# Kernel optimization log

Hardware: AMD Instinct MI355X
Metric: run time of the kernel (lower is better)

Reference implementation:

```python
import jax, jax.numpy as jnp
import numpy as np

D_MODEL = 1024
STATE_DIM = 128


def setup_inputs() -> dict:
    key = jax.random.key(0)
    ks = jax.random.split(key, 8)
    B, T, D, N = 8, 4096, D_MODEL, STATE_DIM
    u = jax.random.normal(ks[0], (B, T, D), dtype=jnp.float32)
    h0 = jnp.zeros((B, N), dtype=jnp.float32)
    log_A = jax.random.normal(ks[1], (N,), dtype=jnp.float32) * 0.1 - 1.0
    B_w = jax.random.normal(ks[2], (N, D), dtype=jnp.float32) / np.sqrt(D)
    B_b = jax.random.normal(ks[3], (N,), dtype=jnp.float32) * 0.01
    C_w = jax.random.normal(ks[4], (D, N), dtype=jnp.float32) / np.sqrt(N)
    C_b = jax.random.normal(ks[5], (D,), dtype=jnp.float32) * 0.01
    D_param = jnp.ones((D,), dtype=jnp.float32) * 0.1
    log_dt = jax.random.normal(ks[6], (N,), dtype=jnp.float32) * 0.1 - 2.0
    return {"u": u, "h0": h0, "log_A": log_A, "B_w": B_w, "B_b": B_b,
            "C_w": C_w, "C_b": C_b, "D_param": D_param, "log_dt": log_dt}


def reference(u, h0, log_A, B_w, B_b, C_w, C_b, D_param, log_dt):
    # u: [B, T, D], h0: [B, N]
    dt = jnp.minimum(jnp.exp(log_dt), 1.0)          # [N]
    A = -jnp.exp(log_A)                             # [N]
    A_bar = jnp.exp(A * dt)                         # [N]
    # B_bar * u, precomputed for all timesteps: [B, T, N]
    Bu = (jnp.einsum('btd,nd->btn', u, B_w) + B_b) * dt

    def step(h, bu_t):
        h = A_bar * h + bu_t                        # [B, N]
        return h, h

    # scan over time: Bu transposed to [T, B, N]
    _, hs = jax.lax.scan(step, h0, jnp.swapaxes(Bu, 0, 1))
    hs = jnp.swapaxes(hs, 0, 1)                     # [B, T, N]
    # y = C h + c_bias + D * u
    y = jnp.einsum('btn,dn->btd', hs, C_w) + C_b + D_param * u
    return y
```

## Files before the change

kernel.cpp:

```cpp
#include <hip/hip_runtime.h>

#define B_SZ 8
#define T_SZ 4096
#define D_SZ 1024
#define N_SZ 128
#define M_SZ (B_SZ*T_SZ)
#define C1 32
#define NC1 (T_SZ/C1)
#define C2 64
#define NC2 (T_SZ/C2)

typedef __attribute__((ext_vector_type(8))) __bf16 bf16x8;
typedef __attribute__((ext_vector_type(4))) float f32x4;
typedef __attribute__((ext_vector_type(4))) unsigned int u32x4;
typedef __attribute__((ext_vector_type(4))) float fvec4;

static __device__ __forceinline__ unsigned short f2bf(float f){
  union { float f; unsigned int u; } v; v.f = f;
  unsigned int r = v.u + 0x7fffu + ((v.u >> 16) & 1u);
  return (unsigned short)(r >> 16);
}

static __device__ __forceinline__ float bf2f(unsigned short s){
  union { unsigned int u; float f; } v; v.u = ((unsigned)s) << 16;
  return v.f;
}

static __device__ __forceinline__ void cp16(const void* g, void* l){
  __builtin_amdgcn_global_load_lds(
      (const __attribute__((address_space(1))) void*)g,
      (__attribute__((address_space(3))) void*)l, 16, 0, 0);
}

static __device__ __forceinline__ f32x4 zero4(){
  f32x4 v = {0.f, 0.f, 0.f, 0.f};
  return v;
}

static __device__ __forceinline__ bf16x8 pack8(fvec4 a, fvec4 b){
  bf16x8 v;
  v[0]=(__bf16)a.x; v[1]=(__bf16)a.y; v[2]=(__bf16)a.z; v[3]=(__bf16)a.w;
  v[4]=(__bf16)b.x; v[5]=(__bf16)b.y; v[6]=(__bf16)b.z; v[7]=(__bf16)b.w;
  return v;
}

__global__ __launch_bounds__(256) void k_conv(const float* __restrict__ Bw,
                                              const float* __restrict__ Cw,
                                              unsigned short* __restrict__ bw,
                                              unsigned short* __restrict__ cw){
  int t = blockIdx.x*256 + threadIdx.x;
  {
    int n = t >> 10, k = t & 1023;
    int c = k >> 6, kk = k & 63;
    unsigned byte = (unsigned)c*16384u + (unsigned)n*128u
                  + (unsigned)((kk*2) ^ ((n&7)<<4));
    bw[byte>>1] = f2bf(Bw[n*1024 + k]);
  }
  {
    int d = t >> 7, k = t & 127;
    int c = d >> 7, dd = d & 127;
    unsigned byte = (unsigned)c*32768u + (unsigned)dd*256u
                  + (unsigned)((k*2) ^ ((dd&15)<<4));
    cw[byte>>1] = f2bf(Cw[d*128 + k]);
  }
}

__global__ __launch_bounds__(256, 4) void k_gemm1c(const float* __restrict__ u,
                                                   const unsigned short* __restrict__ bw,
                                                   const float* __restrict__ Bb,
                                                   const float* __restrict__ logA,
                                                   const float* __restrict__ logdt,
                                                   unsigned short* __restrict__ Bu_bf,
                                                   float* __restrict__ carry){
  __shared__ __align__(16) char smem[20480];
  unsigned short* lA = (unsigned short*)smem;
  unsigned short* lB = (unsigned short*)(smem + 4096);
  float*          BuT = (float*)smem;
  const int tid  = threadIdx.x;
  const int lane = tid & 63;
  const int wave = tid >> 6;
  const int bc   = blockIdx.x;
  const int m0   = bc * 32;
  const int l15  = lane & 15;
  const int lhi  = lane >> 4;
  const int rt   = (wave & 1) * 16;
  const int ct0  = (wave >> 1) * 4;

  f32x4 acc[4];
  #pragma unroll
  for (int i=0;i<4;++i) acc[i] = zero4();

  for (int kc=0; kc<16; ++kc){
    #pragma unroll
    for (int rep=0; rep<4; ++rep){
      const char* g = (const char*)bw + kc*16384 + rep*4096 + tid*16;
      cp16(g, (char*)lB + rep*4096 + tid*16);
    }
    {
      int row = tid >> 3, ks = tid & 7;
      const float* src = u + (size_t)(m0+row)*1024 + kc*64 + ks*8;
      fvec4 f0 = *(const fvec4*)src;
      fvec4 f1 = *(const fvec4*)(src+4);
      unsigned byte = (unsigned)row*128u + (unsigned)((ks*16) ^ ((row&7)<<4));
      *(bf16x8*)((char*)lA + byte) = pack8(f0, f1);
    }
    __syncthreads();
    #pragma unroll
    for (int k0=0; k0<64; k0+=32){
      int arow = rt + l15;
      int ak = k0 + lhi*8;
      bf16x8 af = *(const bf16x8*)((const char*)lA + arow*128 + ((ak*2) ^ ((arow&7)<<4)));
      #pragma unroll
      for (int j=0;j<4;++j){
        int bn = (ct0+j)*16 + l15;
        bf16x8 bfv = *(const bf16x8*)((const char*)lB + bn*128 + ((ak*2) ^ ((bn&7)<<4)));
        acc[j] = __builtin_amdgcn_mfma_f32_16x16x32_bf16(af, bfv, acc[j], 0, 0, 0);
      }
    }
    __syncthreads();
  }

  #pragma unroll
  for (int j=0;j<4;++j){
    int n = (ct0+j)*16 + l15;
    float dt = fminf(__expf(logdt[n]), 1.f);
    float bb = Bb[n];
    #pragma unroll
    for (int r=0;r<4;++r){
      int ml = rt + lhi*4 + r;
      BuT[ml*128 + n] = (acc[j][r] + bb) * dt;
    }
  }
  __syncthreads();

  #pragma unroll
  for (int i=0;i<2;++i){
    int q = i*256 + tid;
    const float* s = BuT + q*8;
    fvec4 a = *(const fvec4*)s;
    fvec4 b = *(const fvec4*)(s+4);
    u32x4 p;
    p.x = (unsigned)f2bf(a.x) | ((unsigned)f2bf(a.y)<<16);
    p.y = (unsigned)f2bf(a.z) | ((unsigned)f2bf(a.w)<<16);
    p.z = (unsigned)f2bf(b.x) | ((unsigned)f2bf(b.y)<<16);
    p.w = (unsigned)f2bf(b.z) | ((unsigned)f2bf(b.w)<<16);
    *(u32x4*)((char*)Bu_bf + (size_t)bc*8192 + (size_t)q*16) = p;
  }

  if (tid < 128){
    int n = tid;
    float dt = fminf(__expf(logdt[n]), 1.f);
    float Ab = __expf(-__expf(logA[n]) * dt);
    float h = 0.f;
    #pragma unroll 8
    for (int j=0;j<C1;++j) h = fmaf(Ab, h, BuT[j*128 + n]);
    carry[(size_t)bc*128 + n] = h;
  }
}

__global__ __launch_bounds__(512, 2) void k_gemm2s(
                                                const unsigned short* __restrict__ Bu_bf,
                                                const float* __restrict__ carry,
                                                const unsigned short* __restrict__ cw,
                                                const float* __restrict__ u,
                                                const float* __restrict__ h0,
                                                const float* __restrict__ Cb,
                                                const float* __restrict__ Dp,
                                                const float* __restrict__ logA,
                                                const float* __restrict__ logdt,
                                                float* __restrict__ y){
  __shared__ __align__(16) unsigned short BuT[64*128];
  __shared__ __align__(16) unsigned short hsT[64*128];
  const int tid = threadIdx.x, lane = tid & 63, wave = tid >> 6;
  const int bc = blockIdx.x;
  const int m0 = bc * 64;
  const int l15 = lane & 15, lhi = lane >> 4;

  #pragma unroll
  for (int i=0;i<2;++i){
    int off = i*8192 + tid*16;
    cp16((const char*)Bu_bf + (size_t)bc*16384 + off, (char*)BuT + off);
  }

  float hreg = 0.f, Ab = 0.f;
  if (tid < 128){
    int n = tid;
    int b = bc >> 6;
    int c32 = (bc & 63) * 2;
    float dt = fminf(__expf(logdt[n]), 1.f);
    float Ad = -__expf(logA[n]) * dt;
    Ab = __expf(Ad);
    float AL = __expf(Ad * (float)C1);
    float h = h0[b*128 + n];
    const float* cp = carry + (size_t)b*NC1*128 + n;
    for (int g=0; g<8; ++g){
      if (g*16 >= c32) break;
      float cbuf[16];
      #pragma unroll
      for (int i=0;i<16;++i) cbuf[i] = cp[(size_t)(g*16+i)*128];
      #pragma unroll
      for (int i=0;i<16;++i){
        int idx = g*16 + i;
        h = (idx < c32) ? fmaf(AL, h, cbuf[i]) : h;
      }
    }
    hreg = h;
  }
  __syncthreads();

  if (tid < 128){
    int n = tid;
    float h = hreg;
    #pragma unroll 8
    for (int j=0;j<C2;++j){
      h = fmaf(Ab, h, bf2f(BuT[j*128 + n]));
      unsigned byte = (unsigned)j*256u + (unsigned)((n*2) ^ ((j&15)<<4));
      *(unsigned short*)((char*)hsT + byte) = f2bf(h);
    }
  }
  __syncthreads();

  const int dn = wave*16 + l15;

  for (int d=0; d<8; ++d){
    const int d0 = d*128;
    const char* cwd = (const char*)cw + (size_t)d*32768;

    bf16x8 bf[4];
    #pragma unroll
    for (int k0i=0;k0i<4;++k0i){
      int ak = k0i*32 + lhi*8;
      bf[k0i] = *(const bf16x8*)(cwd + dn*256 + ((ak*2) ^ ((dn&15)<<4)));
    }

    const int dc = d0 + dn;
    float cb = Cb[dc], dp = Dp[dc];
    float up[4][4];
    #pragma unroll
    for (int mt=0;mt<4;++mt){
      #pragma unroll
      for (int r=0;r<4;++r){
        int m = m0 + mt*16 + lhi*4 + r;
        up[mt][r] = u[(size_t)m*1024 + dc];
      }
    }

    f32x4 acc[4];
    #pragma unroll
    for (int i=0;i<4;++i) acc[i] = zero4();

    #pragma unroll
    for (int k0i=0;k0i<4;++k0i){
      int ak = k0i*32 + lhi*8;
      #pragma unroll
      for (int mt=0;mt<4;++mt){
        int arow = mt*16 + l15;
        bf16x8 af = *(const bf16x8*)((const char*)hsT + arow*256 + ((ak*2) ^ ((arow&15)<<4)));
        acc[mt] = __builtin_amdgcn_mfma_f32_16x16x32_bf16(af, bf[k0i], acc[mt], 0, 0, 0);
      }
    }

    #pragma unroll
    for (int mt=0;mt<4;++mt){
      #pragma unroll
      for (int r=0;r<4;++r){
        int m = m0 + mt*16 + lhi*4 + r;
        size_t off = (size_t)m*1024 + dc;
        y[off] = acc[mt][r] + cb + dp*up[mt][r];
      }
    }
  }
}

extern "C" void kernel_launch(void* const* d_in, const int* in_sizes, int n_in,
                              void* d_out, int out_size, void* d_ws, size_t ws_size,
                              hipStream_t stream){
  (void)in_sizes; (void)n_in; (void)out_size; (void)ws_size;
  const float* u     = (const float*)d_in[0];
  const float* h0    = (const float*)d_in[1];
  const float* logA  = (const float*)d_in[2];
  const float* Bw    = (const float*)d_in[3];
  const float* Bb    = (const float*)d_in[4];
  const float* Cw    = (const float*)d_in[5];
  const float* Cb    = (const float*)d_in[6];
  const float* Dp    = (const float*)d_in[7];
  const float* logdt = (const float*)d_in[8];
  float* y = (float*)d_out;

  char* ws = (char*)d_ws;
  unsigned short* Bu_bf = (unsigned short*)(ws);
  float*          carry = (float*)(ws + 8388608);
  unsigned short* bw    = (unsigned short*)(ws + 8912896);
  unsigned short* cw    = (unsigned short*)(ws + 9175040);

  k_conv  <<<dim3(512),  dim3(256), 0, stream>>>(Bw, Cw, bw, cw);
  k_gemm1c<<<dim3(1024), dim3(256), 0, stream>>>(u, bw, Bb, logA, logdt, Bu_bf, carry);
  k_gemm2s<<<dim3(512),  dim3(512), 0, stream>>>(Bu_bf, carry, cw, u, h0, Cb, Dp,
                                                 logA, logdt, y);
}
```

Measured before the change: 89.56 us.

## Halve k_gemm2s block size and stage C weights in LDS with prefetch

k_gemm2s drops from 512 to 256 threads per block. Each wave now covers 32 output columns (two MFMA column tiles) instead of 16, so each A fragment read from LDS is reused twice. The C-weight slice for each wave is copied into a per-wave LDS buffer with async cp16. The next d-chunk is prefetched after the MFMAs and before the epilogue stores, with a manual vmcnt wait to overlap the load with the output writes. The cost is 32KB more LDS, higher register pressure from doubled accumulators and u values, and a fragile hand-tuned waitcnt.

```diff
diff --git a/kernel.cpp b/kernel.cpp
--- a/kernel.cpp
+++ b/kernel.cpp
@@ -158,7 +158,7 @@
   }
 }
 
-__global__ __launch_bounds__(512, 2) void k_gemm2s(
+__global__ __launch_bounds__(256, 2) void k_gemm2s(
                                                 const unsigned short* __restrict__ Bu_bf,
                                                 const float* __restrict__ carry,
                                                 const unsigned short* __restrict__ cw,
@@ -171,15 +171,22 @@
                                                 float* __restrict__ y){
   __shared__ __align__(16) unsigned short BuT[64*128];
   __shared__ __align__(16) unsigned short hsT[64*128];
+  __shared__ __align__(16) unsigned short cwP[4*32*128];
   const int tid = threadIdx.x, lane = tid & 63, wave = tid >> 6;
   const int bc = blockIdx.x;
   const int m0 = bc * 64;
   const int l15 = lane & 15, lhi = lane >> 4;
-
-  #pragma unroll
-  for (int i=0;i<2;++i){
-    int off = i*8192 + tid*16;
+  char* myP = (char*)cwP + wave*8192;
+
+  #pragma unroll
+  for (int i=0;i<4;++i){
+    int off = i*4096 + tid*16;
     cp16((const char*)Bu_bf + (size_t)bc*16384 + off, (char*)BuT + off);
+  }
+  #pragma unroll
+  for (int i=0;i<8;++i){
+    int off = i*1024 + lane*16;
+    cp16((const char*)cw + wave*8192 + off, myP + off);
   }
 
   float hreg = 0.f, Ab = 0.f;
@@ -220,54 +227,77 @@
   }
   __syncthreads();
 
-  const int dn = wave*16 + l15;
-
   for (int d=0; d<8; ++d){
-    const int d0 = d*128;
-    const char* cwd = (const char*)cw + (size_t)d*32768;
-
-    bf16x8 bf[4];
+    const int dc0 = d*128 + wave*32 + l15;
+
+    float up[2][4][4];
+    #pragma unroll
+    for (int ct=0;ct<2;++ct){
+      int dc = dc0 + ct*16;
+      #pragma unroll
+      for (int mt=0;mt<4;++mt){
+        #pragma unroll
+        for (int r=0;r<4;++r){
+          int m = m0 + mt*16 + lhi*4 + r;
+          up[ct][mt][r] = u[(size_t)m*1024 + dc];
+        }
+      }
+    }
+
+    f32x4 acc[2][4];
+    #pragma unroll
+    for (int i=0;i<2;++i)
+      #pragma unroll
+      for (int j=0;j<4;++j) acc[i][j] = zero4();
+
     #pragma unroll
     for (int k0i=0;k0i<4;++k0i){
       int ak = k0i*32 + lhi*8;
-      bf[k0i] = *(const bf16x8*)(cwd + dn*256 + ((ak*2) ^ ((dn&15)<<4)));
-    }
-
-    const int dc = d0 + dn;
-    float cb = Cb[dc], dp = Dp[dc];
-    float up[4][4];
-    #pragma unroll
-    for (int mt=0;mt<4;++mt){
-      #pragma unroll
-      for (int r=0;r<4;++r){
-        int m = m0 + mt*16 + lhi*4 + r;
-        up[mt][r] = u[(size_t)m*1024 + dc];
-      }
-    }
-
-    f32x4 acc[4];
-    #pragma unroll
-    for (int i=0;i<4;++i) acc[i] = zero4();
-
-    #pragma unroll
-    for (int k0i=0;k0i<4;++k0i){
-      int ak = k0i*32 + lhi*8;
+      bf16x8 bf[2];
+      #pragma unroll
+      for (int ct=0;ct<2;++ct){
+        int rl = ct*16 + l15;
+        bf[ct] = *(const bf16x8*)(myP + rl*256 + ((ak*2) ^ ((rl&15)<<4)));
+      }
       #pragma unroll
       for (int mt=0;mt<4;++mt){
         int arow = mt*16 + l15;
         bf16x8 af = *(const bf16x8*)((const char*)hsT + arow*256 + ((ak*2) ^ ((arow&15)<<4)));
-        acc[mt] = __builtin_amdgcn_mfma_f32_16x16x32_bf16(af, bf[k0i], acc[mt], 0, 0, 0);
-      }
-    }
-
-    #pragma unroll
-    for (int mt=0;mt<4;++mt){
-      #pragma unroll
-      for (int r=0;r<4;++r){
-        int m = m0 + mt*16 + lhi*4 + r;
-        size_t off = (size_t)m*1024 + dc;
-        y[off] = acc[mt][r] + cb + dp*up[mt][r];
-      }
+        #pragma unroll
+        for (int ct=0;ct<2;++ct)
+          acc[ct][mt] = __builtin_amdgcn_mfma_f32_16x16x32_bf16(af, bf[ct],
+                                                                acc[ct][mt], 0, 0, 0);
+      }
+    }
+
+    if (d < 7){
+      __builtin_amdgcn_sched_barrier(0);
+      #pragma unroll
+      for (int i=0;i<8;++i){
+        int off = i*1024 + lane*16;
+        cp16((const char*)cw + (size_t)(d+1)*32768 + wave*8192 + off, myP + off);
+      }
+      __builtin_amdgcn_sched_barrier(0);
+    }
+
+    #pragma unroll
+    for (int ct=0;ct<2;++ct){
+      int dc = dc0 + ct*16;
+      float cb = Cb[dc], dp = Dp[dc];
+      #pragma unroll
+      for (int mt=0;mt<4;++mt){
+        #pragma unroll
+        for (int r=0;r<4;++r){
+          int m = m0 + mt*16 + lhi*4 + r;
+          size_t off = (size_t)m*1024 + dc;
+          y[off] = acc[ct][mt][r] + cb + dp*up[ct][mt][r];
+        }
+      }
+    }
+
+    if (d < 7){
+      asm volatile("s_waitcnt vmcnt(32)" ::: "memory");
+      __builtin_amdgcn_sched_barrier(0);
     }
   }
 }
@@ -295,6 +325,6 @@
 
   k_conv  <<<dim3(512),  dim3(256), 0, stream>>>(Bw, Cw, bw, cw);
   k_gemm1c<<<dim3(1024), dim3(256), 0, stream>>>(u, bw, Bb, logA, logdt, Bu_bf, carry);
-  k_gemm2s<<<dim3(512),  dim3(512), 0, stream>>>(Bu_bf, carry, cw, u, h0, Cb, Dp,
+  k_gemm2s<<<dim3(512),  dim3(256), 0, stream>>>(Bu_bf, carry, cw, u, h0, Cb, Dp,
                                                  logA, logdt, y);
 }
```

New measurement: 86.93 us. 1.03x faster.
